# Performance work log

Measured on AMD Instinct MI355X. Metric: run time of the kernel, lower is better.

## Reference

```python
import jax, jax.numpy as jnp
import numpy as np

N, E = 30000, 480000      # nodes, edges
F, D, H, O = 128, 128, 256, 1  # in feat, embed, encoder hidden, out
ITERS = 5                 # decoder_maxBpIter
EPS = 1e-5                # BatchNorm eps


def _bn(x, gamma, beta):
    # BatchNorm1d in training mode: batch statistics, biased variance
    m = x.mean(0)
    v = x.var(0)
    return (x - m) * jax.lax.rsqrt(v + EPS) * gamma + beta


def _gcn(x, src, dst, W, b):
    # PyG GCNConv: add self-loops, symmetric normalization, scatter-add
    n = x.shape[0]
    loops = jnp.arange(n)
    s = jnp.concatenate([src, loops])
    d = jnp.concatenate([dst, loops])
    deg = jax.ops.segment_sum(jnp.ones(s.shape[0], x.dtype), d, num_segments=n)
    dis = jnp.where(deg > 0, jax.lax.rsqrt(deg), 0.0)
    norm = dis[s] * dis[d]                      # [E+N]
    h = x @ W                                   # [N, D]
    out = jax.ops.segment_sum(h[s] * norm[:, None], d, num_segments=n)
    return out + b


def _gru(inp, hid, W_ih, W_hh, b_ih, b_hh):
    # torch.nn.GRUCell math; gate order r, z, n
    gi = inp @ W_ih.T + b_ih
    gh = hid @ W_hh.T + b_hh
    ir, iz, inn = jnp.split(gi, 3, axis=1)
    hr, hz, hn = jnp.split(gh, 3, axis=1)
    r = jax.nn.sigmoid(ir + hr)
    z = jax.nn.sigmoid(iz + hz)
    nn_ = jnp.tanh(inn + r * hn)
    return (1.0 - z) * nn_ + z * hid


def setup_inputs() -> dict:
    key = jax.random.key(0)
    ks = jax.random.split(key, 12)
    f32 = jnp.float32
    return {
        "x": jax.random.normal(ks[0], (N, F), f32),
        "edge_index": jax.random.randint(ks[1], (2, E), 0, N),
        # decoder.inputLayer
        "W_in": jax.random.normal(ks[2], (F, D), f32) / np.sqrt(F),
        "b_in": jnp.zeros((D,), f32),
        "g0": jnp.ones((D,), f32), "be0": jnp.zeros((D,), f32),
        # GCNConv
        "W_g": jax.random.normal(ks[3], (D, D), f32) / np.sqrt(D),
        "b_g": jnp.zeros((D,), f32),
        # GRUCell
        "W_ih": jax.random.normal(ks[4], (3 * D, D), f32) / np.sqrt(D),
        "W_hh": jax.random.normal(ks[5], (3 * D, D), f32) / np.sqrt(D),
        "b_ih": jnp.zeros((3 * D,), f32),
        "b_hh": jnp.zeros((3 * D,), f32),
        # per-cycle BN, output BN
        "g_c": jnp.ones((D,), f32), "be_c": jnp.zeros((D,), f32),
        "g_o": jnp.ones((D,), f32), "be_o": jnp.zeros((D,), f32),
        # encoder
        "W1": jax.random.normal(ks[6], (D, H), f32) / np.sqrt(D),
        "b1": jnp.zeros((H,), f32),
        "g1": jnp.ones((H,), f32), "be1": jnp.zeros((H,), f32),
        "W2": jax.random.normal(ks[7], (H, O), f32) / np.sqrt(H),
        "b2": jnp.zeros((O,), f32),
    }


def reference(x, edge_index, W_in, b_in, g0, be0, W_g, b_g,
              W_ih, W_hh, b_ih, b_hh, g_c, be_c, g_o, be_o,
              W1, b1, g1, be1, W2, b2):
    src, dst = edge_index[0], edge_index[1]
    # decoder inputLayer: Linear -> LeakyReLU(slope=0, i.e. ReLU) -> BN
    h = _bn(jnp.maximum(x @ W_in + b_in, 0.0), g0, be0)

    def step(carry, _):
        h, mx = carry
        c = _gcn(h, src, dst, W_g, b_g)
        hn = _gru(h, c, W_ih, W_hh, b_ih, b_hh)  # combine(pre_x, conv_out)
        hn = _bn(hn, g_c, be_c)
        return (hn, jnp.maximum(mx, hn)), None

    (_, mx), _ = jax.lax.scan(step, (h, h), None, length=ITERS)
    y = _bn(mx, g_o, be_o)                      # decoder outputLayer BN
    # encoder: Linear -> BN -> LeakyReLU(0); auxFeatDim==0 so no concat
    y = jnp.maximum(_bn(y @ W1 + b1, g1, be1), 0.0)
    return y @ W2 + b2                          # [N, 1]
```

## Files before the change

### kernel.cpp

```cpp
#include <hip/hip_runtime.h>
#include <cmath>

#define EPSBN 1e-5f

typedef __attribute__((ext_vector_type(8))) short short8v;
typedef __attribute__((ext_vector_type(4))) short short4v;
typedef __attribute__((ext_vector_type(4))) float f32x4;

__device__ inline unsigned short f2b(float x) {
  union { float f; unsigned int u; } v; v.f = x;
  unsigned int b = v.u;
  return (unsigned short)((b + 0x7FFFu + ((b >> 16) & 1u)) >> 16);
}
__device__ inline float b2f(unsigned short x) {
  union { unsigned int u; float f; } v; v.u = ((unsigned int)x) << 16;
  return v.f;
}

__global__ __launch_bounds__(256) void k_wprep(const float* __restrict__ W_g, const float* __restrict__ W_ih,
                                               const float* __restrict__ W_hh, const float* __restrict__ W_in,
                                               const float* __restrict__ W1, const float* __restrict__ b_ih,
                                               unsigned short* __restrict__ fusedBT, unsigned short* __restrict__ BThh,
                                               unsigned short* __restrict__ BTin, unsigned short* __restrict__ BT1,
                                               float* __restrict__ fbias, float* __restrict__ stats,
                                               int* __restrict__ degi, int N) {
  int i = blockIdx.x * 256 + threadIdx.x;
  if (i < 16384) {
    int k = i >> 7, m = i & 127;
    fusedBT[m * 128 + k] = f2b(W_g[i]);
  } else if (i < 65536) {
    int j = i - 16384;
    fusedBT[16384 + j] = f2b(W_ih[j]);
  } else if (i < 114688) {
    int j = i - 65536;
    BThh[j] = f2b(W_hh[j]);
  } else if (i < 131072) {
    int j = i - 114688;
    int k = j >> 7, m = j & 127;
    BTin[m * 128 + k] = f2b(W_in[j]);
  } else if (i < 163840) {
    int j = i - 131072;
    int k = j >> 8, m = j & 255;
    BT1[m * 128 + k] = f2b(W1[j]);
  } else if (i < 164352) {
    int j = i - 163840;
    fbias[j] = (j < 128) ? 0.f : b_ih[j - 128];
  } else if (i < 168448) {
    stats[i - 164352] = 0.f;
  } else if (i < 168448 + N) {
    degi[i - 168448] = 0;
  }
}

__global__ __launch_bounds__(256) void k_count_deg(const int* __restrict__ dst, int* __restrict__ deg, int E) {
  int i = blockIdx.x * 256 + threadIdx.x;
  if (i < E) atomicAdd(&deg[dst[i]], 1);
}

__global__ __launch_bounds__(256) void k_scan_p1(const int* __restrict__ deg, int* __restrict__ rowptr,
                                                 int* __restrict__ bsum, float* __restrict__ dis, int N) {
  __shared__ int sd[256];
  int t = threadIdx.x;
  int i = blockIdx.x * 256 + t;
  int v = (i < N) ? deg[i] : 0;
  if (i < N) dis[i] = rsqrtf((float)(v + 1));
  sd[t] = v;
  __syncthreads();
  for (int off = 1; off < 256; off <<= 1) {
    int u = (t >= off) ? sd[t - off] : 0;
    __syncthreads();
    sd[t] += u;
    __syncthreads();
  }
  if (i < N) rowptr[i] = sd[t] - v;
  if (t == 255) bsum[blockIdx.x] = sd[255];
}

__global__ void k_scan_p2(int* __restrict__ bsum, int NBLK) {
  __shared__ int sd[256];
  int t = threadIdx.x;
  int v = (t < NBLK) ? bsum[t] : 0;
  sd[t] = v;
  __syncthreads();
  for (int off = 1; off < 256; off <<= 1) {
    int u = (t >= off) ? sd[t - off] : 0;
    __syncthreads();
    sd[t] += u;
    __syncthreads();
  }
  if (t < NBLK) bsum[t] = sd[t] - v;
}

__global__ __launch_bounds__(256) void k_scan_p3(int* __restrict__ rowptr, int* __restrict__ cursor,
                                                 const int* __restrict__ bsum, int N, int E) {
  int i = blockIdx.x * 256 + threadIdx.x;
  if (i < N) {
    int v = rowptr[i] + bsum[blockIdx.x];
    rowptr[i] = v;
    cursor[i] = v;
  } else if (i == N) {
    rowptr[N] = E;
  }
}

__global__ __launch_bounds__(256) void k_csr_fill(const int* __restrict__ src, const int* __restrict__ dst,
                                                  int* __restrict__ cursor, int* __restrict__ csr_src, int E) {
  int e = blockIdx.x * 256 + threadIdx.x;
  if (e >= E) return;
  int s = src[e], d = dst[e];
  int pos = atomicAdd(&cursor[d], 1);
  csr_src[pos] = s;
}

template<int ABF, int STATS, int SPLIT, int OBF, int BNA>
__global__ __launch_bounds__(256) void k_mmx(const void* __restrict__ Ap, const unsigned short* __restrict__ BT,
                                             const float* __restrict__ bias,
                                             void* __restrict__ Co, unsigned short* __restrict__ Csplit,
                                             const float* __restrict__ coefA,
                                             float* __restrict__ psum, float* __restrict__ psqs,
                                             int N, int ldA, int ldC, int relu)
{
  __shared__ unsigned short As[128 * 128];
  __shared__ unsigned short Bs[128 * 128];
  char* Asb = (char*)As;
  char* Bsb = (char*)Bs;
  int tid = threadIdx.x;
  int brow = blockIdx.y * 128, bcol = blockIdx.x * 128;

#pragma unroll
  for (int p = 0; p < 8; ++p) {
    int idx = p * 256 + tid;
    int r = idx >> 4, ch = idx & 15;
    int arow = brow + r;
    short8v v = {0, 0, 0, 0, 0, 0, 0, 0};
    if (ABF) {
      if (arow < N) v = *(const short8v*)((const unsigned short*)Ap + (size_t)arow * ldA + ch * 8);
      if (BNA) {
#pragma unroll
        for (int j = 0; j < 8; ++j) {
          int k = ch * 8 + j;
          float f = b2f((unsigned short)v[j]) * coefA[k] + coefA[128 + k];
          v[j] = (short)f2b(f);
        }
      }
    } else {
      if (arow < N) {
        const float* a = (const float*)Ap + (size_t)arow * ldA + ch * 8;
        f32x4 x0 = *(const f32x4*)a;
        f32x4 x1 = *(const f32x4*)(a + 4);
        v[0] = (short)f2b(x0[0]); v[1] = (short)f2b(x0[1]);
        v[2] = (short)f2b(x0[2]); v[3] = (short)f2b(x0[3]);
        v[4] = (short)f2b(x1[0]); v[5] = (short)f2b(x1[1]);
        v[6] = (short)f2b(x1[2]); v[7] = (short)f2b(x1[3]);
      }
    }
    *(short8v*)(Asb + r * 256 + ((ch * 16) ^ ((r & 7) << 4))) = v;
  }
#pragma unroll
  for (int p = 0; p < 8; ++p) {
    int idx = p * 256 + tid;
    int r = idx >> 4, ch = idx & 15;
    short8v v = *(const short8v*)(BT + (size_t)(bcol + r) * 128 + ch * 8);
    *(short8v*)(Bsb + r * 256 + ((ch * 16) ^ ((r & 7) << 4))) = v;
  }
  __syncthreads();

  int w = tid >> 6, l = tid & 63;
  int wm = (w >> 1) * 64, wn = (w & 1) * 64;
  int lg = l >> 4, lr = l & 15;
  f32x4 acc[4][4] = {};

#pragma unroll
  for (int ks = 0; ks < 4; ++ks) {
    int kb = ks * 64 + lg * 8;
    short8v a[4], b[4];
#pragma unroll
    for (int mt = 0; mt < 4; ++mt) {
      int r = wm + mt * 16 + lr;
      short4v lo = *(const short4v*)(Asb + r * 256 + (kb ^ ((r & 7) << 4)));
      short4v hi = *(const short4v*)(Asb + r * 256 + ((kb + 32) ^ ((r & 7) << 4)));
      a[mt] = __builtin_shufflevector(lo, hi, 0, 1, 2, 3, 4, 5, 6, 7);
    }
#pragma unroll
    for (int nt = 0; nt < 4; ++nt) {
      int r = wn + nt * 16 + lr;
      short4v lo = *(const short4v*)(Bsb + r * 256 + (kb ^ ((r & 7) << 4)));
      short4v hi = *(const short4v*)(Bsb + r * 256 + ((kb + 32) ^ ((r & 7) << 4)));
      b[nt] = __builtin_shufflevector(lo, hi, 0, 1, 2, 3, 4, 5, 6, 7);
    }
#pragma unroll
    for (int mt = 0; mt < 4; ++mt)
#pragma unroll
      for (int nt = 0; nt < 4; ++nt)
        acc[mt][nt] = __builtin_amdgcn_mfma_f32_16x16x32_bf16(a[mt], b[nt], acc[mt][nt], 0, 0, 0);
  }

  float sc[4] = {0.f, 0.f, 0.f, 0.f}, scc[4] = {0.f, 0.f, 0.f, 0.f};
  bool bfdest = SPLIT && (bcol == 0);
#pragma unroll
  for (int mt = 0; mt < 4; ++mt) {
#pragma unroll
    for (int nt = 0; nt < 4; ++nt) {
      int col = bcol + wn + nt * 16 + lr;
      float bv = bias ? bias[col] : 0.f;
#pragma unroll
      for (int r4 = 0; r4 < 4; ++r4) {
        int row = brow + wm + mt * 16 + lg * 4 + r4;
        if (row < N) {
          float v = acc[mt][nt][r4] + bv;
          if (relu) v = fmaxf(v, 0.f);
          if (bfdest) {
            Csplit[(size_t)row * 128 + col] = f2b(v);
          } else {
            int cc = SPLIT ? (col - 128) : col;
            if (OBF) ((unsigned short*)Co)[(size_t)row * ldC + cc] = f2b(v);
            else ((float*)Co)[(size_t)row * ldC + cc] = v;
          }
          if (STATS) { sc[nt] += v; scc[nt] += v * v; }
        }
      }
    }
  }
  if (STATS) {
#pragma unroll
    for (int nt = 0; nt < 4; ++nt) {
      float s = sc[nt], ss = scc[nt];
      s += __shfl_xor(s, 16); s += __shfl_xor(s, 32);
      ss += __shfl_xor(ss, 16); ss += __shfl_xor(ss, 32);
      if (lg == 0) {
        int col = bcol + wn + nt * 16 + lr;
        atomicAdd(&psum[col], s);
        atomicAdd(&psqs[col], ss);
      }
    }
  }
}

__global__ __launch_bounds__(256) void k_gcn_gather(const int* __restrict__ rowptr, const int* __restrict__ csr_src,
                                                    const float* __restrict__ dis,
                                                    const unsigned short* __restrict__ hp,
                                                    const float* __restrict__ bg,
                                                    float* __restrict__ c, unsigned short* __restrict__ cbf, int N) {
  int t = blockIdx.x * 256 + threadIdx.x;
  int g = t >> 5, lane = t & 31;
  if (g >= N) return;
  int off = lane << 2;
  float dd = dis[g];
  float w0 = dd * dd;
  float4 acc = *(const float4*)(bg + off);
  short4v hv = *(const short4v*)(hp + ((size_t)g << 7) + off);
  acc.x += w0 * b2f((unsigned short)hv[0]);
  acc.y += w0 * b2f((unsigned short)hv[1]);
  acc.z += w0 * b2f((unsigned short)hv[2]);
  acc.w += w0 * b2f((unsigned short)hv[3]);
  int beg = rowptr[g], end = rowptr[g + 1];
  int j = beg;
  for (; j + 3 < end; j += 4) {
    int s0 = csr_src[j], s1 = csr_src[j + 1], s2 = csr_src[j + 2], s3 = csr_src[j + 3];
    float n0 = dis[s0] * dd, n1 = dis[s1] * dd, n2 = dis[s2] * dd, n3 = dis[s3] * dd;
    short4v v0 = *(const short4v*)(hp + ((size_t)s0 << 7) + off);
    short4v v1 = *(const short4v*)(hp + ((size_t)s1 << 7) + off);
    short4v v2 = *(const short4v*)(hp + ((size_t)s2 << 7) + off);
    short4v v3 = *(const short4v*)(hp + ((size_t)s3 << 7) + off);
    acc.x += n0 * b2f((unsigned short)v0[0]) + n1 * b2f((unsigned short)v1[0]) + n2 * b2f((unsigned short)v2[0]) + n3 * b2f((unsigned short)v3[0]);
    acc.y += n0 * b2f((unsigned short)v0[1]) + n1 * b2f((unsigned short)v1[1]) + n2 * b2f((unsigned short)v2[1]) + n3 * b2f((unsigned short)v3[1]);
    acc.z += n0 * b2f((unsigned short)v0[2]) + n1 * b2f((unsigned short)v1[2]) + n2 * b2f((unsigned short)v2[2]) + n3 * b2f((unsigned short)v3[2]);
    acc.w += n0 * b2f((unsigned short)v0[3]) + n1 * b2f((unsigned short)v1[3]) + n2 * b2f((unsigned short)v2[3]) + n3 * b2f((unsigned short)v3[3]);
  }
  for (; j < end; ++j) {
    int s0 = csr_src[j];
    float n0 = dis[s0] * dd;
    short4v v0 = *(const short4v*)(hp + ((size_t)s0 << 7) + off);
    acc.x += n0 * b2f((unsigned short)v0[0]);
    acc.y += n0 * b2f((unsigned short)v0[1]);
    acc.z += n0 * b2f((unsigned short)v0[2]);
    acc.w += n0 * b2f((unsigned short)v0[3]);
  }
  *(float4*)(c + ((size_t)g << 7) + off) = acc;
  short4v b;
  b[0] = (short)f2b(acc.x); b[1] = (short)f2b(acc.y);
  b[2] = (short)f2b(acc.z); b[3] = (short)f2b(acc.w);
  *(short4v*)(cbf + ((size_t)g << 7) + off) = b;
}

__global__ __launch_bounds__(512) void k_gru(const unsigned short* __restrict__ gib,
                                             const unsigned short* __restrict__ ghb,
                                             float* __restrict__ cb,
                                             float* __restrict__ psum, float* __restrict__ psqs, int N) {
  int tx = threadIdx.x & 127, ty = threadIdx.x >> 7;
  int n0 = blockIdx.x * 128;
  float s = 0.f, ss = 0.f;
  for (int r = ty; r < 128; r += 4) {
    int n = n0 + r;
    if (n >= N) break;
    size_t bi = (size_t)n * 384 + tx;
    float ir = b2f(gib[bi]), iz = b2f(gib[bi + 128]), in_ = b2f(gib[bi + 256]);
    float hr = b2f(ghb[bi]), hz = b2f(ghb[bi + 128]), hn_ = b2f(ghb[bi + 256]);
    float cv = cb[(size_t)n * 128 + tx];
    float rr = 1.f / (1.f + expf(-(ir + hr)));
    float z  = 1.f / (1.f + expf(-(iz + hz)));
    float nn = tanhf(in_ + rr * hn_);
    float v = (1.f - z) * nn + z * cv;
    cb[(size_t)n * 128 + tx] = v;
    s += v; ss += v * v;
  }
  __shared__ float sd[2][4][128];
  sd[0][ty][tx] = s; sd[1][ty][tx] = ss;
  __syncthreads();
  if (ty == 0) {
    s  = sd[0][0][tx] + sd[0][1][tx] + sd[0][2][tx] + sd[0][3][tx];
    ss = sd[1][0][tx] + sd[1][1][tx] + sd[1][2][tx] + sd[1][3][tx];
    atomicAdd(&psum[tx], s);
    atomicAdd(&psqs[tx], ss);
  }
}

template<int MODE, int STATS>
__global__ __launch_bounds__(512) void k_bn_apply(const float* __restrict__ x, int ldx,
                                                  const float* __restrict__ psum, const float* __restrict__ psqs,
                                                  const float* __restrict__ gamma, const float* __restrict__ beta,
                                                  float invN,
                                                  unsigned short* __restrict__ yb, unsigned short* __restrict__ mx,
                                                  float* __restrict__ npsum, float* __restrict__ npsqs,
                                                  int N, int R) {
  __shared__ float cA[128], cB[128];
  int t = threadIdx.x;
  if (t < 128) {
    float m = psum[t] * invN;
    float var = psqs[t] * invN - m * m;
    float a = gamma[t] * rsqrtf(var + EPSBN);
    cA[t] = a; cB[t] = beta[t] - m * a;
  }
  __syncthreads();
  int tx = t & 127, ty = t >> 7;
  int n0 = blockIdx.x * R;
  float s = 0.f, ss = 0.f;
  for (int r = ty; r < R; r += 4) {
    int n = n0 + r;
    if (n >= N) break;
    size_t i = (size_t)n * 128 + tx;
    float v = x[(size_t)n * ldx + tx] * cA[tx] + cB[tx];
    float w = v;
    if (MODE == 1) {
      w = fmaxf(b2f(mx[i]), v);
      mx[i] = f2b(w);
    } else {
      mx[i] = f2b(v);
    }
    yb[i] = f2b(v);
    if (STATS) { s += w; ss += w * w; }
  }
  if (STATS) {
    __shared__ float sd[2][4][128];
    sd[0][ty][tx] = s; sd[1][ty][tx] = ss;
    __syncthreads();
    if (ty == 0) {
      for (int q = 1; q < 4; ++q) { s += sd[0][q][tx]; ss += sd[1][q][tx]; }
      atomicAdd(&npsum[tx], s);
      atomicAdd(&npsqs[tx], ss);
    }
  }
}

__global__ void k_coef(const float* __restrict__ psum, const float* __restrict__ psqs,
                       const float* __restrict__ gamma, const float* __restrict__ beta,
                       float invN, float* __restrict__ coef, int D) {
  int t = threadIdx.x;
  if (t < D) {
    float m = psum[t] * invN;
    float var = psqs[t] * invN - m * m;
    float a = gamma[t] * rsqrtf(var + EPSBN);
    coef[t] = a;
    coef[D + t] = beta[t] - m * a;
  }
}

__global__ __launch_bounds__(256) void k_matvec(const unsigned short* __restrict__ y, const float* __restrict__ coef,
                                                const float* __restrict__ W2, const float* __restrict__ b2,
                                                float* __restrict__ out, int N) {
  int t = blockIdx.x * 256 + threadIdx.x;
  int row = t >> 6, lane = t & 63;
  if (row >= N) return;
  const unsigned short* yr = y + (size_t)row * 384;
  float s = 0.f;
#pragma unroll
  for (int k = 0; k < 4; ++k) {
    int c = lane + 64 * k;
    float v = fmaxf(b2f(yr[c]) * coef[c] + coef[256 + c], 0.f);
    s += v * W2[c];
  }
#pragma unroll
  for (int off = 32; off > 0; off >>= 1) s += __shfl_down(s, off);
  if (lane == 0) out[row] = s + b2[0];
}

extern "C" void kernel_launch(void* const* d_in, const int* in_sizes, int n_in,
                              void* d_out, int out_size, void* d_ws, size_t ws_size,
                              hipStream_t stream) {
  const float* x    = (const float*)d_in[0];
  const int*   ei   = (const int*)d_in[1];
  const float* W_in = (const float*)d_in[2];
  const float* b_in = (const float*)d_in[3];
  const float* g0   = (const float*)d_in[4];
  const float* be0  = (const float*)d_in[5];
  const float* W_g  = (const float*)d_in[6];
  const float* b_g  = (const float*)d_in[7];
  const float* W_ih = (const float*)d_in[8];
  const float* W_hh = (const float*)d_in[9];
  const float* b_ih = (const float*)d_in[10];
  const float* b_hh = (const float*)d_in[11];
  const float* g_c  = (const float*)d_in[12];
  const float* be_c = (const float*)d_in[13];
  const float* g_o  = (const float*)d_in[14];
  const float* be_o = (const float*)d_in[15];
  const float* W1   = (const float*)d_in[16];
  const float* b1   = (const float*)d_in[17];
  const float* g1   = (const float*)d_in[18];
  const float* be1  = (const float*)d_in[19];
  const float* W2   = (const float*)d_in[20];
  const float* b2   = (const float*)d_in[21];

  const int N = in_sizes[0] / 128;
  const int E = in_sizes[1] / 2;
  const int ND = N * 128;
  const float invN = 1.0f / (float)N;

  float* p   = (float*)d_ws;
  float* cb  = p; p += ND;
  float* dis = p; p += ((N + 255) & ~255);
  float* stats = p; p += 8 * 512;
  float* fbias = p; p += 512;
  float* coefO = p; p += 256;
  float* coef1 = p; p += 512;
  int*   degi    = (int*)p; p += ((N + 255) & ~255);
  int*   rowptr  = (int*)p; p += ((N + 1 + 255) & ~255);
  int*   cursor  = (int*)p; p += ((N + 255) & ~255);
  int*   bsum    = (int*)p; p += 256;
  int*   csr_src = (int*)p; p += E;
  unsigned short* h_bf    = (unsigned short*)p;
  unsigned short* hp_bf   = h_bf + (size_t)ND;
  unsigned short* cb_bf   = hp_bf + (size_t)ND;
  unsigned short* mx_bf   = cb_bf + (size_t)ND;
  unsigned short* gib_bf  = mx_bf + (size_t)ND;
  unsigned short* ghb_bf  = gib_bf + (size_t)N * 384;
  unsigned short* fusedBT = ghb_bf + (size_t)N * 384;
  unsigned short* BThh    = fusedBT + 512 * 128;
  unsigned short* BTin    = BThh + 384 * 128;
  unsigned short* BT1     = BTin + 128 * 128;

  float* ps0 = stats;
  float* psc[5];
  for (int i = 0; i < 5; ++i) psc[i] = stats + 512 * (1 + i);
  float* pso = stats + 512 * 6;
  float* ps1 = stats + 512 * 7;

  dim3 blk(256);
  int rb = (N + 127) / 128;
  int NBLK = (N + 255) / 256;
  int bnb = (N + 127) / 128;

  k_wprep<<<(168448 + N + 255) / 256, blk, 0, stream>>>(W_g, W_ih, W_hh, W_in, W1, b_ih,
                                                        fusedBT, BThh, BTin, BT1, fbias, stats, degi, N);
  k_count_deg<<<(E + 255) / 256, blk, 0, stream>>>(ei + E, degi, E);
  k_scan_p1<<<NBLK, blk, 0, stream>>>(degi, rowptr, bsum, dis, N);
  k_scan_p2<<<1, blk, 0, stream>>>(bsum, NBLK);
  k_scan_p3<<<(N + 256) / 256, blk, 0, stream>>>(rowptr, cursor, bsum, N, E);
  k_csr_fill<<<(E + 255) / 256, blk, 0, stream>>>(ei, ei + E, cursor, csr_src, E);

  k_mmx<0, 1, 0, 0, 0><<<dim3(1, rb), blk, 0, stream>>>(x, BTin, b_in, cb, nullptr, nullptr,
                                                        ps0, ps0 + 256, N, 128, 128, 1);
  k_bn_apply<3, 0><<<bnb, 512, 0, stream>>>(cb, 128, ps0, ps0 + 256, g0, be0, invN,
                                            h_bf, mx_bf, nullptr, nullptr, N, 128);

  for (int it = 0; it < 5; ++it) {
    k_mmx<1, 0, 1, 1, 0><<<dim3(4, rb), blk, 0, stream>>>(h_bf, fusedBT, fbias, gib_bf, hp_bf, nullptr,
                                                          nullptr, nullptr, N, 128, 384, 0);
    k_gcn_gather<<<(N * 32 + 255) / 256, blk, 0, stream>>>(rowptr, csr_src, dis, hp_bf, b_g, cb, cb_bf, N);
    k_mmx<1, 0, 0, 1, 0><<<dim3(3, rb), blk, 0, stream>>>(cb_bf, BThh, b_hh, ghb_bf, nullptr, nullptr,
                                                          nullptr, nullptr, N, 128, 384, 0);
    k_gru<<<bnb, 512, 0, stream>>>(gib_bf, ghb_bf, cb, psc[it], psc[it] + 256, N);
    if (it < 4)
      k_bn_apply<1, 0><<<bnb, 512, 0, stream>>>(cb, 128, psc[it], psc[it] + 256, g_c, be_c, invN,
                                                h_bf, mx_bf, nullptr, nullptr, N, 128);
    else
      k_bn_apply<1, 1><<<bnb, 512, 0, stream>>>(cb, 128, psc[it], psc[it] + 256, g_c, be_c, invN,
                                                h_bf, mx_bf, pso, pso + 256, N, 128);
  }

  k_coef<<<1, 128, 0, stream>>>(pso, pso + 256, g_o, be_o, invN, coefO, 128);
  k_mmx<1, 1, 0, 1, 1><<<dim3(2, rb), blk, 0, stream>>>(mx_bf, BT1, b1, ghb_bf, nullptr, coefO,
                                                        ps1, ps1 + 256, N, 128, 384, 0);
  k_coef<<<1, 256, 0, stream>>>(ps1, ps1 + 256, g1, be1, invN, coef1, 256);
  k_matvec<<<(N * 64 + 255) / 256, blk, 0, stream>>>(ghb_bf, coef1, W2, b2, (float*)d_out, N);
}
```

Before: 774.1 us.

## Fuse BatchNorm apply and running max into GEMM prologue, finalize stats in last block

Removes the per-iteration k_bn_apply pass by applying the BN affine coefficients while loading fp32 pre-BN activations into the fused GEMM's A tile. Block column 0 of that GEMM also updates the bf16 running-max buffer. The separate k_coef launches are replaced by a last-block-done atomic counter that computes the BN coefficients at the end of the stats-producing kernels. The GEMM now reads fp32 instead of bf16 input, doubling its A-side traffic, and a new cf buffer is added so the gather output and GRU output do not overwrite each other.

```diff
diff --git a/kernel.cpp b/kernel.cpp
--- a/kernel.cpp
+++ b/kernel.cpp
@@ -45,10 +45,10 @@
   } else if (i < 164352) {
     int j = i - 163840;
     fbias[j] = (j < 128) ? 0.f : b_ih[j - 128];
-  } else if (i < 168448) {
+  } else if (i < 168456) {
     stats[i - 164352] = 0.f;
-  } else if (i < 168448 + N) {
-    degi[i - 168448] = 0;
+  } else if (i < 168456 + N) {
+    degi[i - 168456] = 0;
   }
 }
 
@@ -112,12 +112,15 @@
   csr_src[pos] = s;
 }
 
-template<int ABF, int STATS, int SPLIT, int OBF, int BNA>
+template<int ABF, int STATS, int SPLIT, int OBF, int BNA, int MXW, int FIN>
 __global__ __launch_bounds__(256) void k_mmx(const void* __restrict__ Ap, const unsigned short* __restrict__ BT,
                                              const float* __restrict__ bias,
                                              void* __restrict__ Co, unsigned short* __restrict__ Csplit,
-                                             const float* __restrict__ coefA,
+                                             const float* __restrict__ coefA, unsigned short* __restrict__ mxp,
                                              float* __restrict__ psum, float* __restrict__ psqs,
+                                             const float* __restrict__ gamma, const float* __restrict__ beta,
+                                             float* __restrict__ coefOut, int* __restrict__ cnt,
+                                             float invN, int D,
                                              int N, int ldA, int ldC, int relu)
 {
   __shared__ unsigned short As[128 * 128];
@@ -132,28 +135,49 @@
     int idx = p * 256 + tid;
     int r = idx >> 4, ch = idx & 15;
     int arow = brow + r;
-    short8v v = {0, 0, 0, 0, 0, 0, 0, 0};
+    float fv[8];
     if (ABF) {
-      if (arow < N) v = *(const short8v*)((const unsigned short*)Ap + (size_t)arow * ldA + ch * 8);
-      if (BNA) {
-#pragma unroll
-        for (int j = 0; j < 8; ++j) {
-          int k = ch * 8 + j;
-          float f = b2f((unsigned short)v[j]) * coefA[k] + coefA[128 + k];
-          v[j] = (short)f2b(f);
-        }
-      }
+      short8v raw = {0, 0, 0, 0, 0, 0, 0, 0};
+      if (arow < N) raw = *(const short8v*)((const unsigned short*)Ap + (size_t)arow * ldA + ch * 8);
+#pragma unroll
+      for (int j = 0; j < 8; ++j) fv[j] = b2f((unsigned short)raw[j]);
     } else {
       if (arow < N) {
         const float* a = (const float*)Ap + (size_t)arow * ldA + ch * 8;
         f32x4 x0 = *(const f32x4*)a;
         f32x4 x1 = *(const f32x4*)(a + 4);
-        v[0] = (short)f2b(x0[0]); v[1] = (short)f2b(x0[1]);
-        v[2] = (short)f2b(x0[2]); v[3] = (short)f2b(x0[3]);
-        v[4] = (short)f2b(x1[0]); v[5] = (short)f2b(x1[1]);
-        v[6] = (short)f2b(x1[2]); v[7] = (short)f2b(x1[3]);
-      }
-    }
+        fv[0] = x0[0]; fv[1] = x0[1]; fv[2] = x0[2]; fv[3] = x0[3];
+        fv[4] = x1[0]; fv[5] = x1[1]; fv[6] = x1[2]; fv[7] = x1[3];
+      } else {
+#pragma unroll
+        for (int j = 0; j < 8; ++j) fv[j] = 0.f;
+      }
+    }
+    if (BNA) {
+#pragma unroll
+      for (int j = 0; j < 8; ++j) {
+        int k = ch * 8 + j;
+        fv[j] = fv[j] * coefA[k] + coefA[128 + k];
+      }
+    }
+    if (MXW) {
+      if (blockIdx.x == 0 && arow < N) {
+        size_t mi = (size_t)arow * 128 + ch * 8;
+        short8v mo;
+        if (MXW == 2) mo = *(const short8v*)(mxp + mi);
+        short8v mn;
+#pragma unroll
+        for (int j = 0; j < 8; ++j) {
+          float w = fv[j];
+          if (MXW == 2) w = fmaxf(b2f((unsigned short)mo[j]), w);
+          mn[j] = (short)f2b(w);
+        }
+        *(short8v*)(mxp + mi) = mn;
+      }
+    }
+    short8v v;
+#pragma unroll
+    for (int j = 0; j < 8; ++j) v[j] = (short)f2b(fv[j]);
     *(short8v*)(Asb + r * 256 + ((ch * 16) ^ ((r & 7) << 4))) = v;
   }
 #pragma unroll
@@ -231,6 +255,25 @@
         int col = bcol + wn + nt * 16 + lr;
         atomicAdd(&psum[col], s);
         atomicAdd(&psqs[col], ss);
+      }
+    }
+    if (FIN) {
+      __shared__ int lastFlag;
+      __syncthreads();
+      __threadfence();
+      if (tid == 0) {
+        int old = atomicAdd(cnt, 1);
+        lastFlag = (old == (int)(gridDim.x * gridDim.y) - 1) ? 1 : 0;
+      }
+      __syncthreads();
+      if (lastFlag && tid < D) {
+        float s = atomicAdd(&psum[tid], 0.f);
+        float ss = atomicAdd(&psqs[tid], 0.f);
+        float m = s * invN;
+        float var = ss * invN - m * m;
+        float a = gamma[tid] * rsqrtf(var + EPSBN);
+        coefOut[tid] = a;
+        coefOut[D + tid] = beta[tid] - m * a;
       }
     }
   }
@@ -285,8 +328,12 @@
 
 __global__ __launch_bounds__(512) void k_gru(const unsigned short* __restrict__ gib,
                                              const unsigned short* __restrict__ ghb,
+                                             const float* __restrict__ cf,
                                              float* __restrict__ cb,
-                                             float* __restrict__ psum, float* __restrict__ psqs, int N) {
+                                             float* __restrict__ psum, float* __restrict__ psqs,
+                                             const float* __restrict__ gamma, const float* __restrict__ beta,
+                                             float* __restrict__ coefOut, int* __restrict__ cnt,
+                                             float invN, int N) {
   int tx = threadIdx.x & 127, ty = threadIdx.x >> 7;
   int n0 = blockIdx.x * 128;
   float s = 0.f, ss = 0.f;
@@ -296,7 +343,7 @@
     size_t bi = (size_t)n * 384 + tx;
     float ir = b2f(gib[bi]), iz = b2f(gib[bi + 128]), in_ = b2f(gib[bi + 256]);
     float hr = b2f(ghb[bi]), hz = b2f(ghb[bi + 128]), hn_ = b2f(ghb[bi + 256]);
-    float cv = cb[(size_t)n * 128 + tx];
+    float cv = cf[(size_t)n * 128 + tx];
     float rr = 1.f / (1.f + expf(-(ir + hr)));
     float z  = 1.f / (1.f + expf(-(iz + hz)));
     float nn = tanhf(in_ + rr * hn_);
@@ -313,16 +360,35 @@
     atomicAdd(&psum[tx], s);
     atomicAdd(&psqs[tx], ss);
   }
-}
-
-template<int MODE, int STATS>
-__global__ __launch_bounds__(512) void k_bn_apply(const float* __restrict__ x, int ldx,
+  __shared__ int lastFlag;
+  __syncthreads();
+  __threadfence();
+  if (threadIdx.x == 0) {
+    int old = atomicAdd(cnt, 1);
+    lastFlag = (old == (int)gridDim.x - 1) ? 1 : 0;
+  }
+  __syncthreads();
+  if (lastFlag && threadIdx.x < 128) {
+    int t = threadIdx.x;
+    float sm = atomicAdd(&psum[t], 0.f);
+    float sq = atomicAdd(&psqs[t], 0.f);
+    float m = sm * invN;
+    float var = sq * invN - m * m;
+    float a = gamma[t] * rsqrtf(var + EPSBN);
+    coefOut[t] = a;
+    coefOut[128 + t] = beta[t] - m * a;
+  }
+}
+
+__global__ __launch_bounds__(512) void k_bn_final(const float* __restrict__ x,
                                                   const float* __restrict__ psum, const float* __restrict__ psqs,
                                                   const float* __restrict__ gamma, const float* __restrict__ beta,
                                                   float invN,
-                                                  unsigned short* __restrict__ yb, unsigned short* __restrict__ mx,
+                                                  unsigned short* __restrict__ mx,
                                                   float* __restrict__ npsum, float* __restrict__ npsqs,
-                                                  int N, int R) {
+                                                  const float* __restrict__ gammaO, const float* __restrict__ betaO,
+                                                  float* __restrict__ coefOut, int* __restrict__ cnt,
+                                                  int N) {
   __shared__ float cA[128], cB[128];
   int t = threadIdx.x;
   if (t < 128) {
@@ -333,45 +399,43 @@
   }
   __syncthreads();
   int tx = t & 127, ty = t >> 7;
-  int n0 = blockIdx.x * R;
+  int n0 = blockIdx.x * 128;
   float s = 0.f, ss = 0.f;
-  for (int r = ty; r < R; r += 4) {
+  for (int r = ty; r < 128; r += 4) {
     int n = n0 + r;
     if (n >= N) break;
     size_t i = (size_t)n * 128 + tx;
-    float v = x[(size_t)n * ldx + tx] * cA[tx] + cB[tx];
-    float w = v;
-    if (MODE == 1) {
-      w = fmaxf(b2f(mx[i]), v);
-      mx[i] = f2b(w);
-    } else {
-      mx[i] = f2b(v);
-    }
-    yb[i] = f2b(v);
-    if (STATS) { s += w; ss += w * w; }
-  }
-  if (STATS) {
-    __shared__ float sd[2][4][128];
-    sd[0][ty][tx] = s; sd[1][ty][tx] = ss;
-    __syncthreads();
-    if (ty == 0) {
-      for (int q = 1; q < 4; ++q) { s += sd[0][q][tx]; ss += sd[1][q][tx]; }
-      atomicAdd(&npsum[tx], s);
-      atomicAdd(&npsqs[tx], ss);
-    }
-  }
-}
-
-__global__ void k_coef(const float* __restrict__ psum, const float* __restrict__ psqs,
-                       const float* __restrict__ gamma, const float* __restrict__ beta,
-                       float invN, float* __restrict__ coef, int D) {
-  int t = threadIdx.x;
-  if (t < D) {
-    float m = psum[t] * invN;
-    float var = psqs[t] * invN - m * m;
-    float a = gamma[t] * rsqrtf(var + EPSBN);
-    coef[t] = a;
-    coef[D + t] = beta[t] - m * a;
+    float v = x[i] * cA[tx] + cB[tx];
+    float w = fmaxf(b2f(mx[i]), v);
+    mx[i] = f2b(w);
+    s += w; ss += w * w;
+  }
+  __shared__ float sd[2][4][128];
+  sd[0][ty][tx] = s; sd[1][ty][tx] = ss;
+  __syncthreads();
+  if (ty == 0) {
+    s  = sd[0][0][tx] + sd[0][1][tx] + sd[0][2][tx] + sd[0][3][tx];
+    ss = sd[1][0][tx] + sd[1][1][tx] + sd[1][2][tx] + sd[1][3][tx];
+    atomicAdd(&npsum[tx], s);
+    atomicAdd(&npsqs[tx], ss);
+  }
+  __shared__ int lastFlag;
+  __syncthreads();
+  __threadfence();
+  if (threadIdx.x == 0) {
+    int old = atomicAdd(cnt, 1);
+    lastFlag = (old == (int)gridDim.x - 1) ? 1 : 0;
+  }
+  __syncthreads();
+  if (lastFlag && threadIdx.x < 128) {
+    int c = threadIdx.x;
+    float sm = atomicAdd(&npsum[c], 0.f);
+    float sq = atomicAdd(&npsqs[c], 0.f);
+    float m = sm * invN;
+    float var = sq * invN - m * m;
+    float a = gammaO[c] * rsqrtf(var + EPSBN);
+    coefOut[c] = a;
+    coefOut[128 + c] = betaO[c] - m * a;
   }
 }
 
@@ -427,18 +491,17 @@
 
   float* p   = (float*)d_ws;
   float* cb  = p; p += ND;
+  float* cf  = p; p += ND;
   float* dis = p; p += ((N + 255) & ~255);
-  float* stats = p; p += 8 * 512;
+  float* stats = p; p += 8 * 512 + 8;
+  float* coefs = p; p += 2560;
   float* fbias = p; p += 512;
-  float* coefO = p; p += 256;
-  float* coef1 = p; p += 512;
-  int*   degi    = (int*)p; p += ((N + 255) & ~255);
   int*   rowptr  = (int*)p; p += ((N + 1 + 255) & ~255);
   int*   cursor  = (int*)p; p += ((N + 255) & ~255);
   int*   bsum    = (int*)p; p += 256;
+  int*   degi    = (int*)p; p += ((N + 255) & ~255);
   int*   csr_src = (int*)p; p += E;
-  unsigned short* h_bf    = (unsigned short*)p;
-  unsigned short* hp_bf   = h_bf + (size_t)ND;
+  unsigned short* hp_bf   = (unsigned short*)p;
   unsigned short* cb_bf   = hp_bf + (size_t)ND;
   unsigned short* mx_bf   = cb_bf + (size_t)ND;
   unsigned short* gib_bf  = mx_bf + (size_t)ND;
@@ -448,18 +511,24 @@
   unsigned short* BTin    = BThh + 384 * 128;
   unsigned short* BT1     = BTin + 128 * 128;
 
+  int* cnt = (int*)(stats + 8 * 512);
   float* ps0 = stats;
   float* psc[5];
   for (int i = 0; i < 5; ++i) psc[i] = stats + 512 * (1 + i);
   float* pso = stats + 512 * 6;
   float* ps1 = stats + 512 * 7;
+  float* coef0 = coefs;
+  float* coefc[5];
+  for (int i = 0; i < 5; ++i) coefc[i] = coefs + 256 * (1 + i);
+  float* coefO = coefs + 256 * 6;
+  float* coef1 = coefs + 256 * 7;
 
   dim3 blk(256);
   int rb = (N + 127) / 128;
   int NBLK = (N + 255) / 256;
   int bnb = (N + 127) / 128;
 
-  k_wprep<<<(168448 + N + 255) / 256, blk, 0, stream>>>(W_g, W_ih, W_hh, W_in, W1, b_ih,
+  k_wprep<<<(168456 + N + 255) / 256, blk, 0, stream>>>(W_g, W_ih, W_hh, W_in, W1, b_ih,
                                                         fusedBT, BThh, BTin, BT1, fbias, stats, degi, N);
   k_count_deg<<<(E + 255) / 256, blk, 0, stream>>>(ei + E, degi, E);
   k_scan_p1<<<NBLK, blk, 0, stream>>>(degi, rowptr, bsum, dis, N);
@@ -467,29 +536,33 @@
   k_scan_p3<<<(N + 256) / 256, blk, 0, stream>>>(rowptr, cursor, bsum, N, E);
   k_csr_fill<<<(E + 255) / 256, blk, 0, stream>>>(ei, ei + E, cursor, csr_src, E);
 
-  k_mmx<0, 1, 0, 0, 0><<<dim3(1, rb), blk, 0, stream>>>(x, BTin, b_in, cb, nullptr, nullptr,
-                                                        ps0, ps0 + 256, N, 128, 128, 1);
-  k_bn_apply<3, 0><<<bnb, 512, 0, stream>>>(cb, 128, ps0, ps0 + 256, g0, be0, invN,
-                                            h_bf, mx_bf, nullptr, nullptr, N, 128);
+  k_mmx<0, 1, 0, 0, 0, 0, 1><<<dim3(1, rb), blk, 0, stream>>>(
+      x, BTin, b_in, cb, nullptr, nullptr, nullptr,
+      ps0, ps0 + 256, g0, be0, coef0, &cnt[0], invN, 128, N, 128, 128, 1);
 
   for (int it = 0; it < 5; ++it) {
-    k_mmx<1, 0, 1, 1, 0><<<dim3(4, rb), blk, 0, stream>>>(h_bf, fusedBT, fbias, gib_bf, hp_bf, nullptr,
-                                                          nullptr, nullptr, N, 128, 384, 0);
-    k_gcn_gather<<<(N * 32 + 255) / 256, blk, 0, stream>>>(rowptr, csr_src, dis, hp_bf, b_g, cb, cb_bf, N);
-    k_mmx<1, 0, 0, 1, 0><<<dim3(3, rb), blk, 0, stream>>>(cb_bf, BThh, b_hh, ghb_bf, nullptr, nullptr,
-                                                          nullptr, nullptr, N, 128, 384, 0);
-    k_gru<<<bnb, 512, 0, stream>>>(gib_bf, ghb_bf, cb, psc[it], psc[it] + 256, N);
-    if (it < 4)
-      k_bn_apply<1, 0><<<bnb, 512, 0, stream>>>(cb, 128, psc[it], psc[it] + 256, g_c, be_c, invN,
-                                                h_bf, mx_bf, nullptr, nullptr, N, 128);
+    const float* cA = (it == 0) ? coef0 : coefc[it - 1];
+    if (it == 0)
+      k_mmx<0, 0, 1, 1, 1, 1, 0><<<dim3(4, rb), blk, 0, stream>>>(
+          cb, fusedBT, fbias, gib_bf, hp_bf, cA, mx_bf,
+          nullptr, nullptr, nullptr, nullptr, nullptr, nullptr, invN, 128, N, 128, 384, 0);
     else
-      k_bn_apply<1, 1><<<bnb, 512, 0, stream>>>(cb, 128, psc[it], psc[it] + 256, g_c, be_c, invN,
-                                                h_bf, mx_bf, pso, pso + 256, N, 128);
-  }
-
-  k_coef<<<1, 128, 0, stream>>>(pso, pso + 256, g_o, be_o, invN, coefO, 128);
-  k_mmx<1, 1, 0, 1, 1><<<dim3(2, rb), blk, 0, stream>>>(mx_bf, BT1, b1, ghb_bf, nullptr, coefO,
-                                                        ps1, ps1 + 256, N, 128, 384, 0);
-  k_coef<<<1, 256, 0, stream>>>(ps1, ps1 + 256, g1, be1, invN, coef1, 256);
+      k_mmx<0, 0, 1, 1, 1, 2, 0><<<dim3(4, rb), blk, 0, stream>>>(
+          cb, fusedBT, fbias, gib_bf, hp_bf, cA, mx_bf,
+          nullptr, nullptr, nullptr, nullptr, nullptr, nullptr, invN, 128, N, 128, 384, 0);
+    k_gcn_gather<<<(N * 32 + 255) / 256, blk, 0, stream>>>(rowptr, csr_src, dis, hp_bf, b_g, cf, cb_bf, N);
+    k_mmx<1, 0, 0, 1, 0, 0, 0><<<dim3(3, rb), blk, 0, stream>>>(
+        cb_bf, BThh, b_hh, ghb_bf, nullptr, nullptr, nullptr,
+        nullptr, nullptr, nullptr, nullptr, nullptr, nullptr, invN, 128, N, 128, 384, 0);
+    k_gru<<<bnb, 512, 0, stream>>>(gib_bf, ghb_bf, cf, cb,
+                                   psc[it], psc[it] + 256, g_c, be_c,
+                                   coefc[it], &cnt[1 + it], invN, N);
+  }
+
+  k_bn_final<<<bnb, 512, 0, stream>>>(cb, psc[4], psc[4] + 256, g_c, be_c, invN,
+                                      mx_bf, pso, pso + 256, g_o, be_o, coefO, &cnt[6], N);
+  k_mmx<1, 1, 0, 1, 1, 0, 1><<<dim3(2, rb), blk, 0, stream>>>(
+      mx_bf, BT1, b1, ghb_bf, nullptr, coefO, nullptr,
+      ps1, ps1 + 256, g1, be1, coef1, &cnt[7], invN, 256, N, 128, 384, 0);
   k_matvec<<<(N * 64 + 255) / 256, blk, 0, stream>>>(ghb_bf, coef1, W2, b2, (float*)d_out, N);
 }
```

Measured after the change: 962.4 us. +24.3%, slower.
